# Kernel optimization log

Measured on AMD Instinct MI355X. Metric: run time of the kernel, lower is better.

## Reference

```python
import jax, jax.numpy as jnp
import numpy as np

TAU = 2.0          # LIF membrane time constant (tau=2.0 in module)
SG_ALPHA = 4.0     # spikingjelly default Sigmoid surrogate alpha


def lif(x, v_th=1.0):
    """MultiStepLIFNode: leaky-integrate-fire over leading time dim T.
    v <- v + (x - v)/tau ; spike = H(v - v_th) ; hard reset v <- 0 where spiked.
    Surrogate gradient (sigmoid) via straight-through for backward.
    x: [T, ...] -> spikes: [T, ...]
    """
    def step(v, xt):
        v = v + (xt - v) / TAU
        sg = jax.nn.sigmoid(SG_ALPHA * (v - v_th))
        hard = (v >= v_th).astype(xt.dtype)
        spike = jax.lax.stop_gradient(hard - sg) + sg
        # detach_reset=True: reset path does not carry gradient
        v = v * (1.0 - jax.lax.stop_gradient(spike))
        return v, spike
    v0 = jnp.zeros_like(x[0])
    _, s = jax.lax.scan(step, v0, x)
    return s


def bn_c(x, scale, bias):
    """Inference-mode BatchNorm folded to per-channel affine; x: [T,B,C,N]."""
    return x * scale[None, None, :, None] + bias[None, None, :, None]


def setup_inputs() -> dict:
    T, B, C, H, W = 4, 32, 512, 14, 14
    Ch = int(C * 4.0)  # mlp hidden
    key = jax.random.key(0)
    ks = jax.random.split(key, 16)
    std = 0.05
    d = {
        'x': jax.random.normal(ks[0], (T, B, C, H, W), jnp.float32),
        'q_w': jax.random.normal(ks[1], (C, C), jnp.float32) * std,
        'q_bn_s': 1.0 + 0.1 * jax.random.normal(ks[2], (C,), jnp.float32),
        'q_bn_b': 0.1 * jax.random.normal(ks[3], (C,), jnp.float32),
        'k_w': jax.random.normal(ks[4], (C, C), jnp.float32) * std,
        'k_bn_s': 1.0 + 0.1 * jax.random.normal(ks[5], (C,), jnp.float32),
        'k_bn_b': 0.1 * jax.random.normal(ks[6], (C,), jnp.float32),
        'proj_w': jax.random.normal(ks[7], (C, C), jnp.float32) * std,
        'proj_b': 0.1 * jax.random.normal(ks[8], (C,), jnp.float32),
        'proj_bn_s': 1.0 + 0.1 * jax.random.normal(ks[9], (C,), jnp.float32),
        'proj_bn_b': 0.1 * jax.random.normal(ks[10], (C,), jnp.float32),
        'mlp1_w': jax.random.normal(ks[11], (Ch, C), jnp.float32) * std,
        'mlp1_b': 0.1 * jax.random.normal(ks[12], (Ch,), jnp.float32),
        'mlp1_bn_s': 1.0 + 0.1 * jax.random.normal(ks[13], (Ch,), jnp.float32),
        'mlp1_bn_b': 0.1 * jax.random.normal(ks[14], (Ch,), jnp.float32),
        'mlp2_w': jax.random.normal(ks[15], (C, Ch), jnp.float32) * std,
        'mlp2_b': 0.1 * jax.random.normal(jax.random.fold_in(key, 100), (C,), jnp.float32),
        'mlp2_bn_s': 1.0 + 0.1 * jax.random.normal(jax.random.fold_in(key, 101), (C,), jnp.float32),
        'mlp2_bn_b': 0.1 * jax.random.normal(jax.random.fold_in(key, 102), (C,), jnp.float32),
    }
    return d


NUM_HEADS = 8


def reference(x, q_w, q_bn_s, q_bn_b, k_w, k_bn_s, k_bn_b,
              proj_w, proj_b, proj_bn_s, proj_bn_b,
              mlp1_w, mlp1_b, mlp1_bn_s, mlp1_bn_b,
              mlp2_w, mlp2_b, mlp2_bn_s, mlp2_bn_b):
    T, B, C, H, W = x.shape
    N = H * W
    h = NUM_HEADS
    Chd = C // h
    xf = x.reshape(T, B, C, N)

    # ---- Token_QK_Attention ----
    q_sp = lif(bn_c(jnp.einsum('oc,tbcn->tbon', q_w, xf), q_bn_s, q_bn_b))
    k_sp = lif(bn_c(jnp.einsum('oc,tbcn->tbon', k_w, xf), k_bn_s, k_bn_b))
    # per-head channel sum of q spikes: [T,B,h,1,N]
    q_sum = q_sp.reshape(T, B, h, Chd, N).sum(axis=3, keepdims=True)
    attn_sp = lif(q_sum, v_th=0.5)                       # attn_lif, v_threshold=0.5
    x_one = attn_sp * k_sp.reshape(T, B, h, Chd, N)      # spiking multiply
    x_one = x_one.reshape(T, B, C, N)
    p = jnp.einsum('oc,tbcn->tbon', proj_w, x_one) + proj_b[None, None, :, None]
    y = lif(bn_c(p, proj_bn_s, proj_bn_b)).reshape(T, B, C, H, W)
    x = x + y                                            # residual

    # ---- MLP ----
    xf = x.reshape(T, B, C, N)
    h1 = jnp.einsum('oc,tbcn->tbon', mlp1_w, xf) + mlp1_b[None, None, :, None]
    h1 = lif(bn_c(h1, mlp1_bn_s, mlp1_bn_b))
    h2 = jnp.einsum('oc,tbcn->tbon', mlp2_w, h1) + mlp2_b[None, None, :, None]
    h2 = lif(bn_c(h2, mlp2_bn_s, mlp2_bn_b))
    return x + h2.reshape(T, B, C, H, W)
```

## Files before the change

### kernel.cpp

```cpp
#include <hip/hip_runtime.h>
#include <cstdint>

#define NT  4
#define NB  32
#define NC  512
#define NCH 2048
#define NN  196
#define NM  (NB * NN)
#define NH  8

struct GP {
    const float *q_bn_s, *q_bn_b, *k_bn_s, *k_bn_b;
    const float *proj_b, *proj_bn_s, *proj_bn_b;
    const float *mlp1_b, *mlp1_bn_s, *mlp1_bn_b;
    const float *mlp2_b, *mlp2_bn_s, *mlp2_bn_b;
    const float *wqkT, *wprojT, *wmlp1T, *wmlp2T;
    const float *xT;
    float *xy;
    float *v_q, *v_k, *v_y, *v_h1, *v_h2, *v_attn;
    unsigned char *q_sp, *k_sp, *x_one, *h1_sp, *attn_sp;
    float *out;
    int t;
};

__device__ __forceinline__ float lif_step(float z, float v_old, float vth, int& sp) {
    float d = __fsub_rn(z, v_old);
    float h = __fmul_rn(d, 0.5f);
    float v = __fadd_rn(v_old, h);
    sp = (v >= vth) ? 1 : 0;
    return sp ? 0.0f : v;
}

typedef const void __attribute__((address_space(1))) gas_t;
typedef void __attribute__((address_space(3))) las_t;
__device__ __forceinline__ void gl_lds16(const float* g, float* l) {
    __builtin_amdgcn_global_load_lds((gas_t*)g, (las_t*)l, 16, 0, 0);
}


__global__ __launch_bounds__(256) void trw_k(const float* __restrict__ src,
                                             float* __restrict__ dst,
                                             int K, int ldD, int offD) {
    __shared__ float tle[32][33];
    const int c0 = blockIdx.x * 32, o0 = blockIdx.y * 32;
    const int tx = threadIdx.x & 31, ty = threadIdx.x >> 5;
#pragma unroll
    for (int r = 0; r < 4; ++r)
        tle[ty + r * 8][tx] = src[(size_t)(o0 + ty + r * 8) * K + c0 + tx];
    __syncthreads();
#pragma unroll
    for (int r = 0; r < 4; ++r)
        dst[(size_t)(c0 + ty + r * 8) * ldD + offD + o0 + tx] = tle[tx][ty + r * 8];
}

__global__ __launch_bounds__(64) void permx_k(const float* __restrict__ x,
                                              float* __restrict__ xT) {
    const int id = blockIdx.x;
    const int b = id & 31;
    const int c = (id >> 5) & 511;
    const int t = id >> 14;
    const float* s = x + ((size_t)(t * NB + b) * NC + c) * NN;
    float* d = xT + ((size_t)(t * NC + c) * NB + b) * NN;
    for (int n = threadIdx.x; n < NN; n += 64) d[n] = s[n];
}

__global__ __launch_bounds__(256) void attn_k(GP gp) {
    const int m = blockIdx.x * 256 + threadIdx.x;
    const int h = blockIdx.y;
    if (m >= NM) return;
    const unsigned char* q = gp.q_sp + (size_t)h * 64 * NM + m;
    int s = 0;
#pragma unroll 8
    for (int d = 0; d < 64; ++d) s += q[(size_t)d * NM];
    float v = gp.t ? gp.v_attn[(size_t)h * NM + m] : 0.0f;
    int sp;
    v = lif_step((float)s, v, 0.5f, sp);
    gp.v_attn[(size_t)h * NM + m] = v;
    gp.attn_sp[(size_t)h * NM + m] = (unsigned char)sp;
}

__global__ __launch_bounds__(256) void xone_k(GP gp) {
    const int c = blockIdx.y;
    const int m4 = (blockIdx.x * 256 + threadIdx.x) * 4;
    if (m4 >= NM) return;
    const unsigned int kv = *(const unsigned int*)(gp.k_sp + (size_t)c * NM + m4);
    const unsigned int av = *(const unsigned int*)(gp.attn_sp + (size_t)(c >> 6) * NM + m4);
    *(unsigned int*)(gp.x_one + (size_t)c * NM + m4) = kv & av;
}

template <int MODE>
__global__ __launch_bounds__(64) void gemm_lif(GP gp) {
    constexpr bool FUSED = (MODE == 1 || MODE == 3);
    constexpr int K_TOT = (MODE == 3) ? 2048 : 512;
    constexpr int LDA = (MODE == 0) ? 1024 : (MODE == 2) ? 2048 : 512;
    constexpr int BK = FUSED ? 32 : 16;
    constexpr int RN = FUSED ? 4 : 8;
    constexpr int BN = FUSED ? 32 : 64;
    constexpr int XP = FUSED ? 40 : 64;
    constexpr int NIT = K_TOT / BK;

    __shared__ float As[2][BK][64];
    __shared__ float Xs[2][BK][XP];

    const int tid = threadIdx.x;
    const int to = tid & 7;
    const int tn = tid >> 3;
    const int m0 = blockIdx.x * BN;
    const int o0 = blockIdx.y * 64;

    const float* wA = (MODE == 0) ? gp.wqkT : (MODE == 1) ? gp.wprojT
                    : (MODE == 2) ? gp.wmlp1T : gp.wmlp2T;
    const float* xf = (MODE == 0) ? gp.xT + (size_t)gp.t * NC * NM : gp.xy;
    const unsigned char* xu = (MODE == 1) ? gp.x_one : gp.h1_sp;

    uint4 xb = {0, 0, 0, 0};

    auto stage = [&](int buf, int c0) {
#pragma unroll
        for (int r = 0; r < BK / 4; ++r) {
            const float* g = wA + (size_t)(c0 + r * 4 + (tid >> 4)) * LDA + o0 + (tid & 15) * 4;
            gl_lds16(g, &As[buf][r * 4][0]);
        }
        if constexpr (!FUSED) {
#pragma unroll
            for (int r = 0; r < BK / 4; ++r) {
                const float* g = xf + (size_t)(c0 + r * 4 + (tid >> 4)) * NM + m0 + (tid & 15) * 4;
                gl_lds16(g, &Xs[buf][r * 4][0]);
            }
        } else {
            xb = *(const uint4*)(xu + (size_t)(c0 + (tid >> 1)) * NM + m0 + (tid & 1) * 16);
        }
    };

    auto xwrite = [&](int buf) {
        if constexpr (FUSED) {
            const int row = tid >> 1, cb = (tid & 1) * 16;
            float* d = &Xs[buf][row][cb];
            const unsigned int w[4] = {xb.x, xb.y, xb.z, xb.w};
#pragma unroll
            for (int q = 0; q < 4; ++q) {
                float4 f;
                f.x = (float)(unsigned char)(w[q]);
                f.y = (float)(unsigned char)(w[q] >> 8);
                f.z = (float)(unsigned char)(w[q] >> 16);
                f.w = (float)(w[q] >> 24);
                *(float4*)(d + q * 4) = f;
            }
        }
    };

    float acc[8][RN];
#pragma unroll
    for (int i = 0; i < 8; ++i)
#pragma unroll
        for (int j = 0; j < RN; ++j) acc[i][j] = 0.0f;

    stage(0, 0);
    asm volatile("s_waitcnt vmcnt(0)" ::: "memory");
    xwrite(0);

#pragma unroll 1
    for (int it = 0; it < NIT; ++it) {
        const int cur = it & 1;
        const bool more = (it + 1 < NIT);
        if (more) stage(cur ^ 1, (it + 1) * BK);

        const float* as = &As[cur][0][0];
        const float* xs = &Xs[cur][0][0];

        if constexpr (!FUSED) {
            float4 a0[2], a1[2], x0[2], x1[2];
            a0[0] = *(const float4*)(as + to * 8);
            a1[0] = *(const float4*)(as + to * 8 + 4);
            x0[0] = *(const float4*)(xs + tn * 8);
            x1[0] = *(const float4*)(xs + tn * 8 + 4);
#pragma unroll
            for (int kk = 0; kk < BK; ++kk) {
                const int s = kk & 1;
                if (kk + 1 < BK) {
                    const int ns = s ^ 1;
                    a0[ns] = *(const float4*)(as + (kk + 1) * 64 + to * 8);
                    a1[ns] = *(const float4*)(as + (kk + 1) * 64 + to * 8 + 4);
                    x0[ns] = *(const float4*)(xs + (kk + 1) * 64 + tn * 8);
                    x1[ns] = *(const float4*)(xs + (kk + 1) * 64 + tn * 8 + 4);
                }
                const float a[8] = {a0[s].x, a0[s].y, a0[s].z, a0[s].w,
                                    a1[s].x, a1[s].y, a1[s].z, a1[s].w};
                const float xr[8] = {x0[s].x, x0[s].y, x0[s].z, x0[s].w,
                                     x1[s].x, x1[s].y, x1[s].z, x1[s].w};
#pragma unroll
                for (int i = 0; i < 8; ++i)
#pragma unroll
                    for (int j = 0; j < 8; ++j)
                        acc[i][j] = __fadd_rn(acc[i][j], __fmul_rn(a[i], xr[j]));
            }
        } else {
            float4 a0[4], a1[4], x0[4];
#pragma unroll
            for (int p = 0; p < 2; ++p) {
                a0[p] = *(const float4*)(as + p * 64 + to * 8);
                a1[p] = *(const float4*)(as + p * 64 + to * 8 + 4);
                x0[p] = *(const float4*)(xs + p * XP + tn * 4);
            }
#pragma unroll
            for (int kk = 0; kk < BK; ++kk) {
                const int s = kk & 3;
                if (kk + 2 < BK) {
                    const int ps = (kk + 2) & 3;
                    a0[ps] = *(const float4*)(as + (kk + 2) * 64 + to * 8);
                    a1[ps] = *(const float4*)(as + (kk + 2) * 64 + to * 8 + 4);
                    x0[ps] = *(const float4*)(xs + (kk + 2) * XP + tn * 4);
                }
                const float a[8] = {a0[s].x, a0[s].y, a0[s].z, a0[s].w,
                                    a1[s].x, a1[s].y, a1[s].z, a1[s].w};
                const float xr[4] = {x0[s].x, x0[s].y, x0[s].z, x0[s].w};
#pragma unroll
                for (int i = 0; i < 8; ++i)
#pragma unroll
                    for (int j = 0; j < 4; ++j)
                        acc[i][j] = __fmaf_rn(a[i], xr[j], acc[i][j]);
            }
        }
        asm volatile("s_waitcnt vmcnt(0)" ::: "memory");
        if (more) xwrite(cur ^ 1);
    }

    const int mb = m0 + tn * RN;
    if constexpr (MODE == 0) {
        const bool isq = (o0 < NC);
        const float* bs = isq ? gp.q_bn_s : gp.k_bn_s;
        const float* bbv = isq ? gp.q_bn_b : gp.k_bn_b;
        float* vb = isq ? gp.v_q : gp.v_k;
        unsigned char* sb = isq ? gp.q_sp : gp.k_sp;
#pragma unroll
        for (int i = 0; i < 8; ++i) {
            const int oo = (o0 + to * 8 + i) & (NC - 1);
            const float sc = bs[oo], bc = bbv[oo];
            float* vr = vb + (size_t)oo * NM + mb;
            float vv[8];
            if (gp.t) {
                const float4 v0 = *(const float4*)vr, v1 = *(const float4*)(vr + 4);
                vv[0] = v0.x; vv[1] = v0.y; vv[2] = v0.z; vv[3] = v0.w;
                vv[4] = v1.x; vv[5] = v1.y; vv[6] = v1.z; vv[7] = v1.w;
            } else {
#pragma unroll
                for (int j = 0; j < 8; ++j) vv[j] = 0.0f;
            }
            unsigned int pk[2] = {0, 0};
#pragma unroll
            for (int j = 0; j < 8; ++j) {
                const float z = __fadd_rn(__fmul_rn(acc[i][j], sc), bc);
                int sp;
                vv[j] = lif_step(z, vv[j], 1.0f, sp);
                pk[j >> 2] |= (unsigned)sp << ((j & 3) * 8);
            }
            *(float4*)vr = make_float4(vv[0], vv[1], vv[2], vv[3]);
            *(float4*)(vr + 4) = make_float4(vv[4], vv[5], vv[6], vv[7]);
            *(unsigned int*)(sb + (size_t)oo * NM + mb) = pk[0];
            *(unsigned int*)(sb + (size_t)oo * NM + mb + 4) = pk[1];
        }
    } else if constexpr (MODE == 2) {
#pragma unroll
        for (int i = 0; i < 8; ++i) {
            const int o = o0 + to * 8 + i;
            const float bi = gp.mlp1_b[o], sc = gp.mlp1_bn_s[o], bc = gp.mlp1_bn_b[o];
            float* vr = gp.v_h1 + (size_t)o * NM + mb;
            float vv[8];
            if (gp.t) {
                const float4 v0 = *(const float4*)vr, v1 = *(const float4*)(vr + 4);
                vv[0] = v0.x; vv[1] = v0.y; vv[2] = v0.z; vv[3] = v0.w;
                vv[4] = v1.x; vv[5] = v1.y; vv[6] = v1.z; vv[7] = v1.w;
            } else {
#pragma unroll
                for (int j = 0; j < 8; ++j) vv[j] = 0.0f;
            }
            unsigned int pk[2] = {0, 0};
#pragma unroll
            for (int j = 0; j < 8; ++j) {
                const float z = __fadd_rn(__fmul_rn(__fadd_rn(acc[i][j], bi), sc), bc);
                int sp;
                vv[j] = lif_step(z, vv[j], 1.0f, sp);
                pk[j >> 2] |= (unsigned)sp << ((j & 3) * 8);
            }
            *(float4*)vr = make_float4(vv[0], vv[1], vv[2], vv[3]);
            *(float4*)(vr + 4) = make_float4(vv[4], vv[5], vv[6], vv[7]);
            *(unsigned int*)(gp.h1_sp + (size_t)o * NM + mb) = pk[0];
            *(unsigned int*)(gp.h1_sp + (size_t)o * NM + mb + 4) = pk[1];
        }
    } else if constexpr (MODE == 1) {
#pragma unroll
        for (int i = 0; i < 8; ++i) {
            const int o = o0 + to * 8 + i;
            const float bi = gp.proj_b[o], sc = gp.proj_bn_s[o], bc = gp.proj_bn_b[o];
            float* vr = gp.v_y + (size_t)o * NM + mb;
            const float4 vld = gp.t ? *(const float4*)vr : make_float4(0, 0, 0, 0);
            const float4 xv = *(const float4*)(gp.xT + ((size_t)gp.t * NC + o) * NM + mb);
            float vv[4] = {vld.x, vld.y, vld.z, vld.w};
            const float xvv[4] = {xv.x, xv.y, xv.z, xv.w};
            float xyo[4];
#pragma unroll
            for (int j = 0; j < 4; ++j) {
                const float z = __fadd_rn(__fmul_rn(__fadd_rn(acc[i][j], bi), sc), bc);
                int sp;
                vv[j] = lif_step(z, vv[j], 1.0f, sp);
                xyo[j] = __fadd_rn(xvv[j], (float)sp);
            }
            *(float4*)vr = make_float4(vv[0], vv[1], vv[2], vv[3]);
            *(float4*)(gp.xy + (size_t)o * NM + mb) = make_float4(xyo[0], xyo[1], xyo[2], xyo[3]);
        }
    } else {
#pragma unroll
        for (int i = 0; i < 8; ++i) {
            const int o = o0 + to * 8 + i;
            const float bi = gp.mlp2_b[o], sc = gp.mlp2_bn_s[o], bc = gp.mlp2_bn_b[o];
            float* vr = gp.v_h2 + (size_t)o * NM + mb;
            const float4 vld = gp.t ? *(const float4*)vr : make_float4(0, 0, 0, 0);
            const float4 xyv = *(const float4*)(gp.xy + (size_t)o * NM + mb);
            float vv[4] = {vld.x, vld.y, vld.z, vld.w};
            const float xyf[4] = {xyv.x, xyv.y, xyv.z, xyv.w};
#pragma unroll
            for (int j = 0; j < 4; ++j) {
                const float z = __fadd_rn(__fmul_rn(__fadd_rn(acc[i][j], bi), sc), bc);
                int sp;
                vv[j] = lif_step(z, vv[j], 1.0f, sp);
                const int m = mb + j;
                const int b = m / NN;
                const int n = m - b * NN;
                gp.out[(((size_t)gp.t * NB + b) * NC + o) * NN + n] = __fadd_rn(xyf[j], (float)sp);
            }
            *(float4*)vr = make_float4(vv[0], vv[1], vv[2], vv[3]);
        }
    }
}

extern "C" void kernel_launch(void* const* d_in, const int* in_sizes, int n_in,
                              void* d_out, int out_size, void* d_ws, size_t ws_size,
                              hipStream_t stream) {
    const float* x       = (const float*)d_in[0];
    const float* q_w     = (const float*)d_in[1];
    const float* k_w     = (const float*)d_in[4];
    const float* proj_w  = (const float*)d_in[7];
    const float* mlp1_w  = (const float*)d_in[11];
    const float* mlp2_w  = (const float*)d_in[15];

    GP gp;
    gp.q_bn_s = (const float*)d_in[2];  gp.q_bn_b = (const float*)d_in[3];
    gp.k_bn_s = (const float*)d_in[5];  gp.k_bn_b = (const float*)d_in[6];
    gp.proj_b = (const float*)d_in[8];  gp.proj_bn_s = (const float*)d_in[9];  gp.proj_bn_b = (const float*)d_in[10];
    gp.mlp1_b = (const float*)d_in[12]; gp.mlp1_bn_s = (const float*)d_in[13]; gp.mlp1_bn_b = (const float*)d_in[14];
    gp.mlp2_b = (const float*)d_in[16]; gp.mlp2_bn_s = (const float*)d_in[17]; gp.mlp2_bn_b = (const float*)d_in[18];
    gp.out = (float*)d_out;

    char* ws = (char*)d_ws;
    size_t off = 0;
    auto alloc = [&](size_t bytes) -> void* {
        void* r = ws + off;
        off += (bytes + 255) & ~(size_t)255;
        return r;
    };
    float* wqkT   = (float*)alloc((size_t)512 * 1024 * 4);
    float* wprojT = (float*)alloc((size_t)512 * 512 * 4);
    float* wmlp1T = (float*)alloc((size_t)512 * 2048 * 4);
    float* wmlp2T = (float*)alloc((size_t)2048 * 512 * 4);
    float* xT     = (float*)alloc((size_t)NT * NC * NM * 4);
    gp.xy     = (float*)alloc((size_t)NC * NM * 4);
    gp.v_q    = (float*)alloc((size_t)NC * NM * 4);
    gp.v_k    = (float*)alloc((size_t)NC * NM * 4);
    gp.v_y    = (float*)alloc((size_t)NC * NM * 4);
    gp.v_h2   = (float*)alloc((size_t)NC * NM * 4);
    gp.v_h1   = (float*)alloc((size_t)NCH * NM * 4);
    gp.v_attn = (float*)alloc((size_t)NH * NM * 4);
    gp.q_sp   = (unsigned char*)alloc((size_t)NC * NM);
    gp.k_sp   = (unsigned char*)alloc((size_t)NC * NM);
    gp.x_one  = (unsigned char*)alloc((size_t)NC * NM);
    gp.h1_sp  = (unsigned char*)alloc((size_t)NCH * NM);
    gp.attn_sp= (unsigned char*)alloc((size_t)NH * NM);
    gp.wqkT = wqkT; gp.wprojT = wprojT; gp.wmlp1T = wmlp1T; gp.wmlp2T = wmlp2T;
    gp.xT = xT;

    trw_k<<<dim3(16, 16), 256, 0, stream>>>(q_w,    wqkT,   512,  1024, 0);
    trw_k<<<dim3(16, 16), 256, 0, stream>>>(k_w,    wqkT,   512,  1024, 512);
    trw_k<<<dim3(16, 16), 256, 0, stream>>>(proj_w, wprojT, 512,  512,  0);
    trw_k<<<dim3(16, 64), 256, 0, stream>>>(mlp1_w, wmlp1T, 512,  2048, 0);
    trw_k<<<dim3(64, 16), 256, 0, stream>>>(mlp2_w, wmlp2T, 2048, 512,  0);
    permx_k<<<NT * NC * NB, 64, 0, stream>>>(x, xT);

    for (int t = 0; t < NT; ++t) {
        gp.t = t;
        gemm_lif<0><<<dim3(98, 16), 64, 0, stream>>>(gp);
        attn_k<<<dim3(25, NH), 256, 0, stream>>>(gp);
        xone_k<<<dim3(7, NC), 256, 0, stream>>>(gp);
        gemm_lif<1><<<dim3(196, 8), 64, 0, stream>>>(gp);
        gemm_lif<2><<<dim3(98, 32), 64, 0, stream>>>(gp);
        gemm_lif<3><<<dim3(196, 8), 64, 0, stream>>>(gp);
    }
}
```

Baseline: 2.853 ms.

## Use 256-thread four-wave GEMM blocks with 4x4 per-thread tiles

Changes the GEMM+LIF kernel from one wave per block with 8x8 or 8x4 per-thread accumulators to four waves per block, each thread computing a 4x4 tile over a uniform 64x64 output tile. Shared-memory staging is split across the waves and guarded by __syncthreads. The fused modes now use 64-wide tiles, which halves their grid. The aim is more waves per CU and less register pressure, giving better latency hiding. The cost is lower arithmetic intensity per thread (more LDS reads per FMA) and block-wide barriers every K step.

```diff
diff --git a/kernel.cpp b/kernel.cpp
--- a/kernel.cpp
+++ b/kernel.cpp
@@ -89,75 +89,80 @@
 }
 
 template <int MODE>
-__global__ __launch_bounds__(64) void gemm_lif(GP gp) {
+__global__ __launch_bounds__(256) void gemm_lif(GP gp) {
     constexpr bool FUSED = (MODE == 1 || MODE == 3);
     constexpr int K_TOT = (MODE == 3) ? 2048 : 512;
     constexpr int LDA = (MODE == 0) ? 1024 : (MODE == 2) ? 2048 : 512;
     constexpr int BK = FUSED ? 32 : 16;
-    constexpr int RN = FUSED ? 4 : 8;
-    constexpr int BN = FUSED ? 32 : 64;
-    constexpr int XP = FUSED ? 40 : 64;
     constexpr int NIT = K_TOT / BK;
 
     __shared__ float As[2][BK][64];
-    __shared__ float Xs[2][BK][XP];
+    __shared__ float Xs[2][BK][64];
 
     const int tid = threadIdx.x;
-    const int to = tid & 7;
-    const int tn = tid >> 3;
-    const int m0 = blockIdx.x * BN;
+    const int lane = tid & 63;
+    const int wid = tid >> 6;
+    const int to = lane & 15;
+    const int tn = lane >> 4;
+    const int m0 = blockIdx.x * 64;
     const int o0 = blockIdx.y * 64;
+    const int xoff = wid * 16 + tn * 4;
+    const int mb = m0 + xoff;
 
     const float* wA = (MODE == 0) ? gp.wqkT : (MODE == 1) ? gp.wprojT
                     : (MODE == 2) ? gp.wmlp1T : gp.wmlp2T;
     const float* xf = (MODE == 0) ? gp.xT + (size_t)gp.t * NC * NM : gp.xy;
     const unsigned char* xu = (MODE == 1) ? gp.x_one : gp.h1_sp;
 
-    uint4 xb = {0, 0, 0, 0};
+    uint2 xb = {0, 0};
+    const int xrow = tid >> 3;
+    const int xco = (tid & 7) * 8;
 
     auto stage = [&](int buf, int c0) {
-#pragma unroll
-        for (int r = 0; r < BK / 4; ++r) {
-            const float* g = wA + (size_t)(c0 + r * 4 + (tid >> 4)) * LDA + o0 + (tid & 15) * 4;
-            gl_lds16(g, &As[buf][r * 4][0]);
-        }
         if constexpr (!FUSED) {
-#pragma unroll
-            for (int r = 0; r < BK / 4; ++r) {
-                const float* g = xf + (size_t)(c0 + r * 4 + (tid >> 4)) * NM + m0 + (tid & 15) * 4;
-                gl_lds16(g, &Xs[buf][r * 4][0]);
-            }
+            gl_lds16(wA + (size_t)(c0 + wid * 4 + (lane >> 4)) * LDA + o0 + (lane & 15) * 4,
+                     &As[buf][wid * 4][0]);
+            gl_lds16(xf + (size_t)(c0 + wid * 4 + (lane >> 4)) * NM + m0 + (lane & 15) * 4,
+                     &Xs[buf][wid * 4][0]);
         } else {
-            xb = *(const uint4*)(xu + (size_t)(c0 + (tid >> 1)) * NM + m0 + (tid & 1) * 16);
+#pragma unroll
+            for (int r = 0; r < 2; ++r)
+                gl_lds16(wA + (size_t)(c0 + wid * 8 + r * 4 + (lane >> 4)) * LDA + o0 + (lane & 15) * 4,
+                         &As[buf][wid * 8 + r * 4][0]);
+            xb = *(const uint2*)(xu + (size_t)(c0 + xrow) * NM + m0 + xco);
         }
     };
 
-    auto xwrite = [&](int buf) {
+    auto xflush = [&](int buf) {
         if constexpr (FUSED) {
-            const int row = tid >> 1, cb = (tid & 1) * 16;
-            float* d = &Xs[buf][row][cb];
-            const unsigned int w[4] = {xb.x, xb.y, xb.z, xb.w};
-#pragma unroll
-            for (int q = 0; q < 4; ++q) {
-                float4 f;
-                f.x = (float)(unsigned char)(w[q]);
-                f.y = (float)(unsigned char)(w[q] >> 8);
-                f.z = (float)(unsigned char)(w[q] >> 16);
-                f.w = (float)(w[q] >> 24);
-                *(float4*)(d + q * 4) = f;
-            }
+            float* d = &Xs[buf][xrow][xco];
+            const unsigned int w0 = xb.x, w1 = xb.y;
+            float4 f0, f1;
+            f0.x = (float)(unsigned char)(w0);
+            f0.y = (float)(unsigned char)(w0 >> 8);
+            f0.z = (float)(unsigned char)(w0 >> 16);
+            f0.w = (float)(w0 >> 24);
+            f1.x = (float)(unsigned char)(w1);
+            f1.y = (float)(unsigned char)(w1 >> 8);
+            f1.z = (float)(unsigned char)(w1 >> 16);
+            f1.w = (float)(w1 >> 24);
+            *(float4*)(d) = f0;
+            *(float4*)(d + 4) = f1;
         }
     };
 
-    float acc[8][RN];
-#pragma unroll
-    for (int i = 0; i < 8; ++i)
-#pragma unroll
-        for (int j = 0; j < RN; ++j) acc[i][j] = 0.0f;
+    float acc[4][4];
+#pragma unroll
+    for (int i = 0; i < 4; ++i)
+#pragma unroll
+        for (int j = 0; j < 4; ++j) acc[i][j] = 0.0f;
 
     stage(0, 0);
-    asm volatile("s_waitcnt vmcnt(0)" ::: "memory");
-    xwrite(0);
+    if constexpr (FUSED) {
+        asm volatile("s_waitcnt vmcnt(0)" ::: "memory");
+        xflush(0);
+    }
+    __syncthreads();
 
 #pragma unroll 1
     for (int it = 0; it < NIT; ++it) {
@@ -168,64 +173,34 @@
         const float* as = &As[cur][0][0];
         const float* xs = &Xs[cur][0][0];
 
-        if constexpr (!FUSED) {
-            float4 a0[2], a1[2], x0[2], x1[2];
-            a0[0] = *(const float4*)(as + to * 8);
-            a1[0] = *(const float4*)(as + to * 8 + 4);
-            x0[0] = *(const float4*)(xs + tn * 8);
-            x1[0] = *(const float4*)(xs + tn * 8 + 4);
-#pragma unroll
-            for (int kk = 0; kk < BK; ++kk) {
-                const int s = kk & 1;
-                if (kk + 1 < BK) {
-                    const int ns = s ^ 1;
-                    a0[ns] = *(const float4*)(as + (kk + 1) * 64 + to * 8);
-                    a1[ns] = *(const float4*)(as + (kk + 1) * 64 + to * 8 + 4);
-                    x0[ns] = *(const float4*)(xs + (kk + 1) * 64 + tn * 8);
-                    x1[ns] = *(const float4*)(xs + (kk + 1) * 64 + tn * 8 + 4);
+        float4 af[2], xv[2];
+        af[0] = *(const float4*)(as + to * 4);
+        xv[0] = *(const float4*)(xs + xoff);
+#pragma unroll
+        for (int kk = 0; kk < BK; ++kk) {
+            const int s = kk & 1;
+            if (kk + 1 < BK) {
+                af[s ^ 1] = *(const float4*)(as + (kk + 1) * 64 + to * 4);
+                xv[s ^ 1] = *(const float4*)(xs + (kk + 1) * 64 + xoff);
+            }
+            const float a4[4] = {af[s].x, af[s].y, af[s].z, af[s].w};
+            const float x4[4] = {xv[s].x, xv[s].y, xv[s].z, xv[s].w};
+#pragma unroll
+            for (int i = 0; i < 4; ++i)
+#pragma unroll
+                for (int j = 0; j < 4; ++j) {
+                    if (FUSED) acc[i][j] = __fmaf_rn(a4[i], x4[j], acc[i][j]);
+                    else       acc[i][j] = __fadd_rn(acc[i][j], __fmul_rn(a4[i], x4[j]));
                 }
-                const float a[8] = {a0[s].x, a0[s].y, a0[s].z, a0[s].w,
-                                    a1[s].x, a1[s].y, a1[s].z, a1[s].w};
-                const float xr[8] = {x0[s].x, x0[s].y, x0[s].z, x0[s].w,
-                                     x1[s].x, x1[s].y, x1[s].z, x1[s].w};
-#pragma unroll
-                for (int i = 0; i < 8; ++i)
-#pragma unroll
-                    for (int j = 0; j < 8; ++j)
-                        acc[i][j] = __fadd_rn(acc[i][j], __fmul_rn(a[i], xr[j]));
-            }
-        } else {
-            float4 a0[4], a1[4], x0[4];
-#pragma unroll
-            for (int p = 0; p < 2; ++p) {
-                a0[p] = *(const float4*)(as + p * 64 + to * 8);
-                a1[p] = *(const float4*)(as + p * 64 + to * 8 + 4);
-                x0[p] = *(const float4*)(xs + p * XP + tn * 4);
-            }
-#pragma unroll
-            for (int kk = 0; kk < BK; ++kk) {
-                const int s = kk & 3;
-                if (kk + 2 < BK) {
-                    const int ps = (kk + 2) & 3;
-                    a0[ps] = *(const float4*)(as + (kk + 2) * 64 + to * 8);
-                    a1[ps] = *(const float4*)(as + (kk + 2) * 64 + to * 8 + 4);
-                    x0[ps] = *(const float4*)(xs + (kk + 2) * XP + tn * 4);
-                }
-                const float a[8] = {a0[s].x, a0[s].y, a0[s].z, a0[s].w,
-                                    a1[s].x, a1[s].y, a1[s].z, a1[s].w};
-                const float xr[4] = {x0[s].x, x0[s].y, x0[s].z, x0[s].w};
-#pragma unroll
-                for (int i = 0; i < 8; ++i)
-#pragma unroll
-                    for (int j = 0; j < 4; ++j)
-                        acc[i][j] = __fmaf_rn(a[i], xr[j], acc[i][j]);
-            }
-        }
-        asm volatile("s_waitcnt vmcnt(0)" ::: "memory");
-        if (more) xwrite(cur ^ 1);
+        }
+
+        if constexpr (FUSED) {
+            asm volatile("s_waitcnt vmcnt(0)" ::: "memory");
+            if (more) xflush(cur ^ 1);
+        }
+        __syncthreads();
     }
 
-    const int mb = m0 + tn * RN;
     if constexpr (MODE == 0) {
         const bool isq = (o0 < NC);
         const float* bs = isq ? gp.q_bn_s : gp.k_bn_s;
@@ -233,70 +208,52 @@
         float* vb = isq ? gp.v_q : gp.v_k;
         unsigned char* sb = isq ? gp.q_sp : gp.k_sp;
 #pragma unroll
-        for (int i = 0; i < 8; ++i) {
-            const int oo = (o0 + to * 8 + i) & (NC - 1);
+        for (int i = 0; i < 4; ++i) {
+            const int oo = (o0 + to * 4 + i) & (NC - 1);
             const float sc = bs[oo], bc = bbv[oo];
             float* vr = vb + (size_t)oo * NM + mb;
-            float vv[8];
-            if (gp.t) {
-                const float4 v0 = *(const float4*)vr, v1 = *(const float4*)(vr + 4);
-                vv[0] = v0.x; vv[1] = v0.y; vv[2] = v0.z; vv[3] = v0.w;
-                vv[4] = v1.x; vv[5] = v1.y; vv[6] = v1.z; vv[7] = v1.w;
-            } else {
-#pragma unroll
-                for (int j = 0; j < 8; ++j) vv[j] = 0.0f;
-            }
-            unsigned int pk[2] = {0, 0};
-#pragma unroll
-            for (int j = 0; j < 8; ++j) {
+            float4 vld = gp.t ? *(const float4*)vr : make_float4(0, 0, 0, 0);
+            float vv[4] = {vld.x, vld.y, vld.z, vld.w};
+            unsigned int pk = 0;
+#pragma unroll
+            for (int j = 0; j < 4; ++j) {
                 const float z = __fadd_rn(__fmul_rn(acc[i][j], sc), bc);
                 int sp;
                 vv[j] = lif_step(z, vv[j], 1.0f, sp);
-                pk[j >> 2] |= (unsigned)sp << ((j & 3) * 8);
+                pk |= (unsigned)sp << (j * 8);
             }
             *(float4*)vr = make_float4(vv[0], vv[1], vv[2], vv[3]);
-            *(float4*)(vr + 4) = make_float4(vv[4], vv[5], vv[6], vv[7]);
-            *(unsigned int*)(sb + (size_t)oo * NM + mb) = pk[0];
-            *(unsigned int*)(sb + (size_t)oo * NM + mb + 4) = pk[1];
+            *(unsigned int*)(sb + (size_t)oo * NM + mb) = pk;
         }
     } else if constexpr (MODE == 2) {
 #pragma unroll
-        for (int i = 0; i < 8; ++i) {
-            const int o = o0 + to * 8 + i;
+        for (int i = 0; i < 4; ++i) {
+            const int o = o0 + to * 4 + i;
             const float bi = gp.mlp1_b[o], sc = gp.mlp1_bn_s[o], bc = gp.mlp1_bn_b[o];
             float* vr = gp.v_h1 + (size_t)o * NM + mb;
-            float vv[8];
-            if (gp.t) {
-                const float4 v0 = *(const float4*)vr, v1 = *(const float4*)(vr + 4);
-                vv[0] = v0.x; vv[1] = v0.y; vv[2] = v0.z; vv[3] = v0.w;
-                vv[4] = v1.x; vv[5] = v1.y; vv[6] = v1.z; vv[7] = v1.w;
-            } else {
-#pragma unroll
-                for (int j = 0; j < 8; ++j) vv[j] = 0.0f;
-            }
-            unsigned int pk[2] = {0, 0};
-#pragma unroll
-            for (int j = 0; j < 8; ++j) {
+            float4 vld = gp.t ? *(const float4*)vr : make_float4(0, 0, 0, 0);
+            float vv[4] = {vld.x, vld.y, vld.z, vld.w};
+            unsigned int pk = 0;
+#pragma unroll
+            for (int j = 0; j < 4; ++j) {
                 const float z = __fadd_rn(__fmul_rn(__fadd_rn(acc[i][j], bi), sc), bc);
                 int sp;
                 vv[j] = lif_step(z, vv[j], 1.0f, sp);
-                pk[j >> 2] |= (unsigned)sp << ((j & 3) * 8);
+                pk |= (unsigned)sp << (j * 8);
             }
             *(float4*)vr = make_float4(vv[0], vv[1], vv[2], vv[3]);
-            *(float4*)(vr + 4) = make_float4(vv[4], vv[5], vv[6], vv[7]);
-            *(unsigned int*)(gp.h1_sp + (size_t)o * NM + mb) = pk[0];
-            *(unsigned int*)(gp.h1_sp + (size_t)o * NM + mb + 4) = pk[1];
+            *(unsigned int*)(gp.h1_sp + (size_t)o * NM + mb) = pk;
         }
     } else if constexpr (MODE == 1) {
 #pragma unroll
-        for (int i = 0; i < 8; ++i) {
-            const int o = o0 + to * 8 + i;
+        for (int i = 0; i < 4; ++i) {
+            const int o = o0 + to * 4 + i;
             const float bi = gp.proj_b[o], sc = gp.proj_bn_s[o], bc = gp.proj_bn_b[o];
             float* vr = gp.v_y + (size_t)o * NM + mb;
             const float4 vld = gp.t ? *(const float4*)vr : make_float4(0, 0, 0, 0);
-            const float4 xv = *(const float4*)(gp.xT + ((size_t)gp.t * NC + o) * NM + mb);
+            const float4 xv4 = *(const float4*)(gp.xT + ((size_t)gp.t * NC + o) * NM + mb);
             float vv[4] = {vld.x, vld.y, vld.z, vld.w};
-            const float xvv[4] = {xv.x, xv.y, xv.z, xv.w};
+            const float xvv[4] = {xv4.x, xv4.y, xv4.z, xv4.w};
             float xyo[4];
 #pragma unroll
             for (int j = 0; j < 4; ++j) {
@@ -310,8 +267,8 @@
         }
     } else {
 #pragma unroll
-        for (int i = 0; i < 8; ++i) {
-            const int o = o0 + to * 8 + i;
+        for (int i = 0; i < 4; ++i) {
+            const int o = o0 + to * 4 + i;
             const float bi = gp.mlp2_b[o], sc = gp.mlp2_bn_s[o], bc = gp.mlp2_bn_b[o];
             float* vr = gp.v_h2 + (size_t)o * NM + mb;
             const float4 vld = gp.t ? *(const float4*)vr : make_float4(0, 0, 0, 0);
@@ -387,11 +344,11 @@
 
     for (int t = 0; t < NT; ++t) {
         gp.t = t;
-        gemm_lif<0><<<dim3(98, 16), 64, 0, stream>>>(gp);
+        gemm_lif<0><<<dim3(98, 16), 256, 0, stream>>>(gp);
         attn_k<<<dim3(25, NH), 256, 0, stream>>>(gp);
         xone_k<<<dim3(7, NC), 256, 0, stream>>>(gp);
-        gemm_lif<1><<<dim3(196, 8), 64, 0, stream>>>(gp);
-        gemm_lif<2><<<dim3(98, 32), 64, 0, stream>>>(gp);
-        gemm_lif<3><<<dim3(196, 8), 64, 0, stream>>>(gp);
+        gemm_lif<1><<<dim3(98, 8), 256, 0, stream>>>(gp);
+        gemm_lif<2><<<dim3(98, 32), 256, 0, stream>>>(gp);
+        gemm_lif<3><<<dim3(98, 8), 256, 0, stream>>>(gp);
     }
 }
```

Result: slower. 3.382 ms (+18.6%).

## Halve output-channel tile in GEMM-LIF kernels and simplify LDS pipeline

Applied to the files above, without the earlier changes.

Shrinks each single-wave block's output tile from 64 to 32 channels, so each thread holds a 4xRN accumulator instead of 8xRN. This doubles the grid and cuts register pressure, aiming for more resident waves to hide latency. It also replaces the manual register double-buffered LDS reads with a simpler unrolled loop, uses BK=16 for the fused modes with narrower spike-byte loads, and vectorises the final output store. In exchange, each weight and activation element is reused less, so total global and LDS traffic goes up.

```diff
diff --git a/kernel.cpp b/kernel.cpp
--- a/kernel.cpp
+++ b/kernel.cpp
@@ -36,6 +36,12 @@
 __device__ __forceinline__ void gl_lds16(const float* g, float* l) {
     __builtin_amdgcn_global_load_lds((gas_t*)g, (las_t*)l, 16, 0, 0);
 }
+__device__ __forceinline__ void vm0() {
+    asm volatile("s_waitcnt vmcnt(0)" ::: "memory");
+}
+__device__ __forceinline__ void lgkm0() {
+    asm volatile("s_waitcnt lgkmcnt(0)" ::: "memory");
+}
 
 
 __global__ __launch_bounds__(256) void trw_k(const float* __restrict__ src,
@@ -93,148 +99,134 @@
     constexpr bool FUSED = (MODE == 1 || MODE == 3);
     constexpr int K_TOT = (MODE == 3) ? 2048 : 512;
     constexpr int LDA = (MODE == 0) ? 1024 : (MODE == 2) ? 2048 : 512;
-    constexpr int BK = FUSED ? 32 : 16;
+    constexpr int BK = 16;
+    constexpr int NIT = K_TOT / BK;
+    constexpr int MT = FUSED ? 32 : 64;
     constexpr int RN = FUSED ? 4 : 8;
-    constexpr int BN = FUSED ? 32 : 64;
-    constexpr int XP = FUSED ? 40 : 64;
-    constexpr int NIT = K_TOT / BK;
-
-    __shared__ float As[2][BK][64];
-    __shared__ float Xs[2][BK][XP];
-
-    const int tid = threadIdx.x;
-    const int to = tid & 7;
-    const int tn = tid >> 3;
-    const int m0 = blockIdx.x * BN;
-    const int o0 = blockIdx.y * 64;
+
+    __shared__ float As[2][BK][32];
+    __shared__ float Xs[2][BK][MT];
+
+    const int lane = threadIdx.x;
+    const int to = lane & 7;
+    const int tn = lane >> 3;
+    const int m0 = blockIdx.x * MT;
+    const int ot = blockIdx.y;
+    const int o0 = ot * 32;
+    const int mb = m0 + tn * RN;
 
     const float* wA = (MODE == 0) ? gp.wqkT : (MODE == 1) ? gp.wprojT
                     : (MODE == 2) ? gp.wmlp1T : gp.wmlp2T;
     const float* xf = (MODE == 0) ? gp.xT + (size_t)gp.t * NC * NM : gp.xy;
     const unsigned char* xu = (MODE == 1) ? gp.x_one : gp.h1_sp;
 
-    uint4 xb = {0, 0, 0, 0};
-
-    auto stage = [&](int buf, int c0) {
-#pragma unroll
-        for (int r = 0; r < BK / 4; ++r) {
-            const float* g = wA + (size_t)(c0 + r * 4 + (tid >> 4)) * LDA + o0 + (tid & 15) * 4;
-            gl_lds16(g, &As[buf][r * 4][0]);
-        }
+    auto stageA = [&](int buf, int s) {
+#pragma unroll
+        for (int r = 0; r < 2; ++r)
+            gl_lds16(wA + (size_t)(s * BK + r * 8 + (lane >> 3)) * LDA + o0 + (lane & 7) * 4,
+                     &As[buf][r * 8][0]);
+    };
+    auto stageXf = [&](int buf, int s) {
+#pragma unroll
+        for (int r = 0; r < 4; ++r)
+            gl_lds16(xf + (size_t)(s * BK + r * 4 + (lane >> 4)) * NM + m0 + (lane & 15) * 4,
+                     &Xs[buf][r * 4][0]);
+    };
+    const int xrow = lane >> 2;
+    const int xcb = (lane & 3) * 8;
+    auto loadB = [&](int s) -> uint2 {
+        return *(const uint2*)(xu + (size_t)(s * BK + xrow) * NM + m0 + xcb);
+    };
+    auto flushB = [&](int buf, uint2 xb) {
+        float* d = &Xs[buf][xrow][xcb];
+        float4 f0, f1;
+        f0.x = (float)(unsigned char)(xb.x);
+        f0.y = (float)(unsigned char)(xb.x >> 8);
+        f0.z = (float)(unsigned char)(xb.x >> 16);
+        f0.w = (float)(xb.x >> 24);
+        f1.x = (float)(unsigned char)(xb.y);
+        f1.y = (float)(unsigned char)(xb.y >> 8);
+        f1.z = (float)(unsigned char)(xb.y >> 16);
+        f1.w = (float)(xb.y >> 24);
+        *(float4*)d = f0;
+        *(float4*)(d + 4) = f1;
+    };
+
+    float acc[4][RN];
+#pragma unroll
+    for (int i = 0; i < 4; ++i)
+#pragma unroll
+        for (int j = 0; j < RN; ++j) acc[i][j] = 0.0f;
+
+    auto compute = [&](int cur) {
         if constexpr (!FUSED) {
-#pragma unroll
-            for (int r = 0; r < BK / 4; ++r) {
-                const float* g = xf + (size_t)(c0 + r * 4 + (tid >> 4)) * NM + m0 + (tid & 15) * 4;
-                gl_lds16(g, &Xs[buf][r * 4][0]);
+#pragma unroll 4
+            for (int kk = 0; kk < BK; ++kk) {
+                const float4 av = *(const float4*)&As[cur][kk][to * 4];
+                const float4 x0 = *(const float4*)&Xs[cur][kk][tn * 8];
+                const float4 x1 = *(const float4*)&Xs[cur][kk][tn * 8 + 4];
+                const float a4[4] = {av.x, av.y, av.z, av.w};
+                const float x8[8] = {x0.x, x0.y, x0.z, x0.w, x1.x, x1.y, x1.z, x1.w};
+#pragma unroll
+                for (int i = 0; i < 4; ++i)
+#pragma unroll
+                    for (int j = 0; j < 8; ++j)
+                        acc[i][j] = __fadd_rn(acc[i][j], __fmul_rn(a4[i], x8[j]));
             }
         } else {
-            xb = *(const uint4*)(xu + (size_t)(c0 + (tid >> 1)) * NM + m0 + (tid & 1) * 16);
-        }
-    };
-
-    auto xwrite = [&](int buf) {
-        if constexpr (FUSED) {
-            const int row = tid >> 1, cb = (tid & 1) * 16;
-            float* d = &Xs[buf][row][cb];
-            const unsigned int w[4] = {xb.x, xb.y, xb.z, xb.w};
-#pragma unroll
-            for (int q = 0; q < 4; ++q) {
-                float4 f;
-                f.x = (float)(unsigned char)(w[q]);
-                f.y = (float)(unsigned char)(w[q] >> 8);
-                f.z = (float)(unsigned char)(w[q] >> 16);
-                f.w = (float)(w[q] >> 24);
-                *(float4*)(d + q * 4) = f;
-            }
-        }
-    };
-
-    float acc[8][RN];
-#pragma unroll
-    for (int i = 0; i < 8; ++i)
-#pragma unroll
-        for (int j = 0; j < RN; ++j) acc[i][j] = 0.0f;
-
-    stage(0, 0);
-    asm volatile("s_waitcnt vmcnt(0)" ::: "memory");
-    xwrite(0);
+#pragma unroll 8
+            for (int kk = 0; kk < BK; ++kk) {
+                const float4 av = *(const float4*)&As[cur][kk][to * 4];
+                const float4 xv = *(const float4*)&Xs[cur][kk][tn * 4];
+                const float a4[4] = {av.x, av.y, av.z, av.w};
+                const float x4[4] = {xv.x, xv.y, xv.z, xv.w};
+#pragma unroll
+                for (int i = 0; i < 4; ++i)
+#pragma unroll
+                    for (int j = 0; j < 4; ++j)
+                        acc[i][j] = __fmaf_rn(a4[i], x4[j], acc[i][j]);
+            }
+        }
+    };
+
+    if constexpr (!FUSED) {
+        stageA(0, 0); stageXf(0, 0);
+        vm0();
+    } else {
+        stageA(0, 0);
+        uint2 xb = loadB(0);
+        vm0();
+        flushB(0, xb);
+        lgkm0();
+    }
 
 #pragma unroll 1
     for (int it = 0; it < NIT; ++it) {
         const int cur = it & 1;
+        const int nxt = cur ^ 1;
         const bool more = (it + 1 < NIT);
-        if (more) stage(cur ^ 1, (it + 1) * BK);
-
-        const float* as = &As[cur][0][0];
-        const float* xs = &Xs[cur][0][0];
-
         if constexpr (!FUSED) {
-            float4 a0[2], a1[2], x0[2], x1[2];
-            a0[0] = *(const float4*)(as + to * 8);
-            a1[0] = *(const float4*)(as + to * 8 + 4);
-            x0[0] = *(const float4*)(xs + tn * 8);
-            x1[0] = *(const float4*)(xs + tn * 8 + 4);
-#pragma unroll
-            for (int kk = 0; kk < BK; ++kk) {
-                const int s = kk & 1;
-                if (kk + 1 < BK) {
-                    const int ns = s ^ 1;
-                    a0[ns] = *(const float4*)(as + (kk + 1) * 64 + to * 8);
-                    a1[ns] = *(const float4*)(as + (kk + 1) * 64 + to * 8 + 4);
-                    x0[ns] = *(const float4*)(xs + (kk + 1) * 64 + tn * 8);
-                    x1[ns] = *(const float4*)(xs + (kk + 1) * 64 + tn * 8 + 4);
-                }
-                const float a[8] = {a0[s].x, a0[s].y, a0[s].z, a0[s].w,
-                                    a1[s].x, a1[s].y, a1[s].z, a1[s].w};
-                const float xr[8] = {x0[s].x, x0[s].y, x0[s].z, x0[s].w,
-                                     x1[s].x, x1[s].y, x1[s].z, x1[s].w};
-#pragma unroll
-                for (int i = 0; i < 8; ++i)
-#pragma unroll
-                    for (int j = 0; j < 8; ++j)
-                        acc[i][j] = __fadd_rn(acc[i][j], __fmul_rn(a[i], xr[j]));
-            }
+            if (more) { stageA(nxt, it + 1); stageXf(nxt, it + 1); }
+            compute(cur);
+            if (more) vm0();
         } else {
-            float4 a0[4], a1[4], x0[4];
-#pragma unroll
-            for (int p = 0; p < 2; ++p) {
-                a0[p] = *(const float4*)(as + p * 64 + to * 8);
-                a1[p] = *(const float4*)(as + p * 64 + to * 8 + 4);
-                x0[p] = *(const float4*)(xs + p * XP + tn * 4);
-            }
-#pragma unroll
-            for (int kk = 0; kk < BK; ++kk) {
-                const int s = kk & 3;
-                if (kk + 2 < BK) {
-                    const int ps = (kk + 2) & 3;
-                    a0[ps] = *(const float4*)(as + (kk + 2) * 64 + to * 8);
-                    a1[ps] = *(const float4*)(as + (kk + 2) * 64 + to * 8 + 4);
-                    x0[ps] = *(const float4*)(xs + (kk + 2) * XP + tn * 4);
-                }
-                const float a[8] = {a0[s].x, a0[s].y, a0[s].z, a0[s].w,
-                                    a1[s].x, a1[s].y, a1[s].z, a1[s].w};
-                const float xr[4] = {x0[s].x, x0[s].y, x0[s].z, x0[s].w};
-#pragma unroll
-                for (int i = 0; i < 8; ++i)
-#pragma unroll
-                    for (int j = 0; j < 4; ++j)
-                        acc[i][j] = __fmaf_rn(a[i], xr[j], acc[i][j]);
-            }
-        }
-        asm volatile("s_waitcnt vmcnt(0)" ::: "memory");
-        if (more) xwrite(cur ^ 1);
+            uint2 xb = {0, 0};
+            if (more) { stageA(nxt, it + 1); xb = loadB(it + 1); }
+            compute(cur);
+            if (more) { vm0(); flushB(nxt, xb); lgkm0(); }
+        }
     }
 
-    const int mb = m0 + tn * RN;
     if constexpr (MODE == 0) {
-        const bool isq = (o0 < NC);
+        const bool isq = (ot < 16);
         const float* bs = isq ? gp.q_bn_s : gp.k_bn_s;
         const float* bbv = isq ? gp.q_bn_b : gp.k_bn_b;
         float* vb = isq ? gp.v_q : gp.v_k;
         unsigned char* sb = isq ? gp.q_sp : gp.k_sp;
-#pragma unroll
-        for (int i = 0; i < 8; ++i) {
-            const int oo = (o0 + to * 8 + i) & (NC - 1);
+        const int ob = (ot & 15) * 32;
+#pragma unroll
+        for (int i = 0; i < 4; ++i) {
+            const int oo = ob + to * 4 + i;
             const float sc = bs[oo], bc = bbv[oo];
             float* vr = vb + (size_t)oo * NM + mb;
             float vv[8];
@@ -260,9 +252,10 @@
             *(unsigned int*)(sb + (size_t)oo * NM + mb + 4) = pk[1];
         }
     } else if constexpr (MODE == 2) {
-#pragma unroll
-        for (int i = 0; i < 8; ++i) {
-            const int o = o0 + to * 8 + i;
+        const int ob = ot * 32;
+#pragma unroll
+        for (int i = 0; i < 4; ++i) {
+            const int o = ob + to * 4 + i;
             const float bi = gp.mlp1_b[o], sc = gp.mlp1_bn_s[o], bc = gp.mlp1_bn_b[o];
             float* vr = gp.v_h1 + (size_t)o * NM + mb;
             float vv[8];
@@ -288,15 +281,16 @@
             *(unsigned int*)(gp.h1_sp + (size_t)o * NM + mb + 4) = pk[1];
         }
     } else if constexpr (MODE == 1) {
-#pragma unroll
-        for (int i = 0; i < 8; ++i) {
-            const int o = o0 + to * 8 + i;
+        const int ob = ot * 32;
+#pragma unroll
+        for (int i = 0; i < 4; ++i) {
+            const int o = ob + to * 4 + i;
             const float bi = gp.proj_b[o], sc = gp.proj_bn_s[o], bc = gp.proj_bn_b[o];
             float* vr = gp.v_y + (size_t)o * NM + mb;
             const float4 vld = gp.t ? *(const float4*)vr : make_float4(0, 0, 0, 0);
-            const float4 xv = *(const float4*)(gp.xT + ((size_t)gp.t * NC + o) * NM + mb);
+            const float4 xv4 = *(const float4*)(gp.xT + ((size_t)gp.t * NC + o) * NM + mb);
             float vv[4] = {vld.x, vld.y, vld.z, vld.w};
-            const float xvv[4] = {xv.x, xv.y, xv.z, xv.w};
+            const float xvv[4] = {xv4.x, xv4.y, xv4.z, xv4.w};
             float xyo[4];
 #pragma unroll
             for (int j = 0; j < 4; ++j) {
@@ -309,25 +303,28 @@
             *(float4*)(gp.xy + (size_t)o * NM + mb) = make_float4(xyo[0], xyo[1], xyo[2], xyo[3]);
         }
     } else {
-#pragma unroll
-        for (int i = 0; i < 8; ++i) {
-            const int o = o0 + to * 8 + i;
+        const int ob = ot * 32;
+        const int b = mb / NN;
+        const int n = mb - b * NN;
+#pragma unroll
+        for (int i = 0; i < 4; ++i) {
+            const int o = ob + to * 4 + i;
             const float bi = gp.mlp2_b[o], sc = gp.mlp2_bn_s[o], bc = gp.mlp2_bn_b[o];
             float* vr = gp.v_h2 + (size_t)o * NM + mb;
             const float4 vld = gp.t ? *(const float4*)vr : make_float4(0, 0, 0, 0);
             const float4 xyv = *(const float4*)(gp.xy + (size_t)o * NM + mb);
             float vv[4] = {vld.x, vld.y, vld.z, vld.w};
             const float xyf[4] = {xyv.x, xyv.y, xyv.z, xyv.w};
+            float ov[4];
 #pragma unroll
             for (int j = 0; j < 4; ++j) {
                 const float z = __fadd_rn(__fmul_rn(__fadd_rn(acc[i][j], bi), sc), bc);
                 int sp;
                 vv[j] = lif_step(z, vv[j], 1.0f, sp);
-                const int m = mb + j;
-                const int b = m / NN;
-                const int n = m - b * NN;
-                gp.out[(((size_t)gp.t * NB + b) * NC + o) * NN + n] = __fadd_rn(xyf[j], (float)sp);
-            }
+                ov[j] = __fadd_rn(xyf[j], (float)sp);
+            }
+            *(float4*)&gp.out[(((size_t)gp.t * NB + b) * NC + o) * NN + n] =
+                make_float4(ov[0], ov[1], ov[2], ov[3]);
             *(float4*)vr = make_float4(vv[0], vv[1], vv[2], vv[3]);
         }
     }
@@ -387,11 +384,11 @@
 
     for (int t = 0; t < NT; ++t) {
         gp.t = t;
-        gemm_lif<0><<<dim3(98, 16), 64, 0, stream>>>(gp);
+        gemm_lif<0><<<dim3(98, 32), 64, 0, stream>>>(gp);
         attn_k<<<dim3(25, NH), 256, 0, stream>>>(gp);
         xone_k<<<dim3(7, NC), 256, 0, stream>>>(gp);
-        gemm_lif<1><<<dim3(196, 8), 64, 0, stream>>>(gp);
-        gemm_lif<2><<<dim3(98, 32), 64, 0, stream>>>(gp);
-        gemm_lif<3><<<dim3(196, 8), 64, 0, stream>>>(gp);
+        gemm_lif<1><<<dim3(196, 16), 64, 0, stream>>>(gp);
+        gemm_lif<2><<<dim3(98, 64), 64, 0, stream>>>(gp);
+        gemm_lif<3><<<dim3(196, 16), 64, 0, stream>>>(gp);
     }
 }
```

Result: faster. 2.586 ms (-9.3%).
